# Kernel optimization log

Hardware: AMD Instinct MI355X
Metric: run time of the kernel (lower is better)

Reference implementation:

```python
import jax, jax.numpy as jnp
import numpy as np

B, T, D, H = 32, 2048, 512, 1024


def setup_inputs() -> dict:
    key = jax.random.key(0)
    ks = jax.random.split(key, 8)
    s = 1.0 / np.sqrt(H)  # torch nn.LSTM init scale
    x = jax.random.normal(ks[0], (B, T, D), jnp.float32)
    lengths = jnp.maximum(jax.random.randint(ks[1], (B,), 0, T), 1).astype(jnp.int32)
    h0 = jax.random.normal(ks[2], (1, B, H), jnp.float32)
    c0 = jax.random.normal(ks[3], (1, B, H), jnp.float32)
    W_ih = jax.random.uniform(ks[4], (4 * H, D), jnp.float32, -s, s)
    W_hh = jax.random.uniform(ks[5], (4 * H, H), jnp.float32, -s, s)
    b_ih = jax.random.uniform(ks[6], (4 * H,), jnp.float32, -s, s)
    b_hh = jax.random.uniform(ks[7], (4 * H,), jnp.float32, -s, s)
    return {"x": x, "lengths": lengths, "h0": h0, "c0": c0,
            "W_ih": W_ih, "W_hh": W_hh, "b_ih": b_ih, "b_hh": b_hh}


def _lstm_final(x, lengths, h0, c0, W_ih, W_hh, b_ih, b_hh):
    # Packed-sequence LSTM: final state per sequence == state at its last valid step.
    # Equivalent masked scan: freeze (h, c) once t >= length.
    t_len = x.shape[1]
    xt = jnp.swapaxes(x, 0, 1)                           # [T, B, D]
    mask = jnp.arange(t_len)[:, None] < lengths[None, :]  # [T, B]
    bias = b_ih + b_hh                                   # [4H]

    def step(carry, inp):
        h, c = carry                                     # [B, H] each
        xb, m = inp                                      # [B, D], [B]
        gates = xb @ W_ih.T + h @ W_hh.T + bias          # [B, 4H]
        i, f, g, o = jnp.split(gates, 4, axis=-1)        # torch gate order i,f,g,o
        c_new = jax.nn.sigmoid(f) * c + jax.nn.sigmoid(i) * jnp.tanh(g)
        h_new = jax.nn.sigmoid(o) * jnp.tanh(c_new)
        m = m[:, None]
        return (jnp.where(m, h_new, h), jnp.where(m, c_new, c)), None

    (h, c), _ = jax.lax.scan(step, (h0[0], c0[0]), (xt, mask))
    return h[None], c[None]                              # [1, B, H] each


def reference(x, lengths, h0, c0, W_ih, W_hh, b_ih, b_hh):
    return _lstm_final(x, lengths, h0, c0, W_ih, W_hh, b_ih, b_hh)
```

## Files before the change

kernel.cpp:

```cpp
#include <hip/hip_runtime.h>
#include <hip/hip_bf16.h>

#define B_ 32
#define T_ 2048
#define D_ 512
#define H_ 1024
#define G4_ 4096
#define NBLK 128
#define JPB 8
#define FSTRIDE 16

typedef __attribute__((ext_vector_type(8))) short short8;
typedef __attribute__((ext_vector_type(4))) float f32x4;
typedef __attribute__((ext_vector_type(4))) int i32x4;

__device__ __forceinline__ float sigmoidf_(float x) { return 1.0f / (1.0f + __expf(-x)); }
__device__ __forceinline__ float tanhf_(float x) {
  float e = __expf(2.0f * x);
  return 1.0f - 2.0f / (e + 1.0f);
}
__device__ __forceinline__ float bf16bits_to_f(unsigned short u) {
  return __builtin_bit_cast(float, (unsigned int)u << 16);
}
__device__ __forceinline__ unsigned short f_to_bf16bits(float f) {
  __hip_bfloat16 h = __float2bfloat16(f);
  return __builtin_bit_cast(unsigned short, h);
}

__device__ __forceinline__ i32x4 load16_sys(const void* p) {
  i32x4 v;
  asm volatile("global_load_dwordx4 %0, %1, off sc0 sc1" : "=v"(v) : "v"(p));
  return v;
}

__global__ __launch_bounds__(256) void xw_gemm(const float* __restrict__ x,
                                               const float* __restrict__ Wih,
                                               __hip_bfloat16* __restrict__ xg,
                                               int t0) {
  __shared__ __align__(16) __hip_bfloat16 As[128][40];
  __shared__ __align__(16) __hip_bfloat16 Bs[128][40];
  __shared__ __align__(16) __hip_bfloat16 Cs[128][132];

  const int tid = threadIdx.x;
  const int bx = blockIdx.x;
  const int by = blockIdx.y;
  const int lane = tid & 63, wave = tid >> 6;
  const int wm = wave >> 1, wn = wave & 1;
  const int lr = lane & 15, kq = (lane >> 4) * 8;

  const int r  = tid >> 1, ks = (tid & 1) * 16;
  const int rowA = by * 128 + r;
  const int bb = rowA & 31, tg = t0 + (rowA >> 5);
  const float* aptr = x  + ((size_t)bb * T_ + tg) * D_ + ks;
  const float* bptr = Wih + (size_t)(bx * 128 + r) * D_ + ks;

  f32x4 acc[4][4];
#pragma unroll
  for (int i = 0; i < 4; ++i)
#pragma unroll
    for (int jj = 0; jj < 4; ++jj) acc[i][jj] = (f32x4){0.f, 0.f, 0.f, 0.f};

  for (int k0 = 0; k0 < D_; k0 += 32) {
    __hip_bfloat16 ta[16], tb[16];
#pragma unroll
    for (int q = 0; q < 4; ++q) {
      f32x4 va = ((const f32x4*)(aptr + k0))[q];
      f32x4 vb = ((const f32x4*)(bptr + k0))[q];
#pragma unroll
      for (int e = 0; e < 4; ++e) {
        ta[q * 4 + e] = __float2bfloat16(va[e]);
        tb[q * 4 + e] = __float2bfloat16(vb[e]);
      }
    }
    __syncthreads();
    *(short8*)&As[r][ks]     = *(const short8*)&ta[0];
    *(short8*)&As[r][ks + 8] = *(const short8*)&ta[8];
    *(short8*)&Bs[r][ks]     = *(const short8*)&tb[0];
    *(short8*)&Bs[r][ks + 8] = *(const short8*)&tb[8];
    __syncthreads();

    short8 af[4], bf[4];
#pragma unroll
    for (int mi = 0; mi < 4; ++mi) af[mi] = *(const short8*)&As[wm * 64 + mi * 16 + lr][kq];
#pragma unroll
    for (int ni = 0; ni < 4; ++ni) bf[ni] = *(const short8*)&Bs[wn * 64 + ni * 16 + lr][kq];
#pragma unroll
    for (int mi = 0; mi < 4; ++mi)
#pragma unroll
      for (int ni = 0; ni < 4; ++ni)
        acc[mi][ni] = __builtin_amdgcn_mfma_f32_16x16x32_bf16(af[mi], bf[ni], acc[mi][ni], 0, 0, 0);
  }

#pragma unroll
  for (int mi = 0; mi < 4; ++mi)
#pragma unroll
    for (int ni = 0; ni < 4; ++ni)
#pragma unroll
      for (int rr = 0; rr < 4; ++rr)
        Cs[wm * 64 + mi * 16 + (lane >> 4) * 4 + rr][wn * 64 + ni * 16 + lr] =
            __float2bfloat16(acc[mi][ni][rr]);
  __syncthreads();

  const int orow = tid >> 1, oseg = (tid & 1) * 64;
  __hip_bfloat16* dst = xg + (size_t)(by * 128 + orow) * G4_ + bx * 128 + oseg;
#pragma unroll
  for (int c2 = 0; c2 < 8; ++c2)
    *(short8*)(dst + c2 * 8) = *(const short8*)&Cs[orow][oseg + c2 * 8];
}

__global__ __launch_bounds__(256, 1) void lstm_rec(
    const __hip_bfloat16* __restrict__ xg, const float* __restrict__ Whh,
    const int* __restrict__ lengths, const float* __restrict__ h0,
    const float* __restrict__ c0, const float* __restrict__ bih,
    const float* __restrict__ bhh, __hip_bfloat16* hbuf,
    float* __restrict__ hstate, float* __restrict__ cstate,
    int* flags, float* __restrict__ out,
    int t0, int t1, int isfirst, int islast) {
  __shared__ float Gs[4][32][36];

  const int g = blockIdx.x, tid = threadIdx.x;
  const int lane = tid & 63, w = tid >> 6;
  const int lr = lane & 15, q = lane >> 4, kq = q * 8;
  const int kkb = w * 8;

  short8 wf[2][8];
#pragma unroll
  for (int ni = 0; ni < 2; ++ni) {
    const int n2 = ni * 16 + lr;
    const int gcol = (n2 >> 3) * H_ + g * JPB + (n2 & 7);
    const float* wbase = Whh + (size_t)gcol * H_ + kq;
#pragma unroll
    for (int kk2 = 0; kk2 < 8; ++kk2) {
      const int k0 = (kkb + kk2) * 32;
      f32x4 w0 = *(const f32x4*)(wbase + k0);
      f32x4 w1 = *(const f32x4*)(wbase + k0 + 4);
      __hip_bfloat16 tw_[8];
#pragma unroll
      for (int e = 0; e < 4; ++e) { tw_[e] = __float2bfloat16(w0[e]); tw_[4 + e] = __float2bfloat16(w1[e]); }
      wf[ni][kk2] = *(const short8*)&tw_[0];
    }
  }

  const int bb2 = (tid & 127) >> 2, j2 = (tid & 3) * 2;
  const int jglob = g * JPB + j2;
  const int len_b = (tid < 128) ? lengths[bb2] : 0;
  int maxlen = 0;
  for (int p = 0; p < B_; ++p) maxlen = max(maxlen, lengths[p]);
  const int tend = min(t1, maxlen);

  float hreg[2], creg[2], bias[4][2];
  if (tid < 128) {
    if (isfirst) {
#pragma unroll
      for (int e = 0; e < 2; ++e) { hreg[e] = h0[bb2 * H_ + jglob + e]; creg[e] = c0[bb2 * H_ + jglob + e]; }
    } else {
#pragma unroll
      for (int e = 0; e < 2; ++e) { hreg[e] = hstate[bb2 * H_ + jglob + e]; creg[e] = cstate[bb2 * H_ + jglob + e]; }
    }
#pragma unroll
    for (int p = 0; p < 4; ++p)
#pragma unroll
      for (int e = 0; e < 2; ++e)
        bias[p][e] = bih[p * H_ + jglob + e] + bhh[p * H_ + jglob + e];
  }

  unsigned long long* hbuf64 = (unsigned long long*)hbuf;
  const int* myflag = &flags[(w * 32 + (lane & 31)) * FSTRIDE];
  const int pw64 = bb2 * (H_ / 4) + g * 2 + ((tid & 3) >> 1);

  for (int t = t0; t < tend; ++t) {
    unsigned int xp[4];
    if (tid < 128) {
      const __hip_bfloat16* xgrow = xg + ((size_t)(t - t0) * B_ + bb2) * G4_ + jglob;
#pragma unroll
      for (int p = 0; p < 4; ++p) xp[p] = *(const unsigned int*)(xgrow + p * H_);
    }

    while (true) {
      int f = __hip_atomic_load(myflag, __ATOMIC_RELAXED, __HIP_MEMORY_SCOPE_AGENT);
      if (__all(f >= t)) break;
      __builtin_amdgcn_s_sleep(1);
    }

    const char* hb = (const char*)(hbuf + (size_t)(t & 1) * (B_ * H_));
    i32x4 raw[2][8];
#pragma unroll
    for (int mi = 0; mi < 2; ++mi) {
      const char* rowp = hb + (size_t)(mi * 16 + lr) * (H_ * 2) + kkb * 64 + q * 16;
#pragma unroll
      for (int kk2 = 0; kk2 < 8; ++kk2)
        raw[mi][kk2] = load16_sys(rowp + kk2 * 64);
    }
    asm volatile("s_waitcnt vmcnt(0)" ::: "memory");
    __builtin_amdgcn_sched_barrier(0);

    short8 af[2][8];
#pragma unroll
    for (int mi = 0; mi < 2; ++mi)
#pragma unroll
      for (int kk2 = 0; kk2 < 8; ++kk2) {
        union { i32x4 i; short8 s; } cv;
        cv.i = raw[mi][kk2];
        af[mi][kk2] = cv.s;
      }

    f32x4 acc[2][2];
#pragma unroll
    for (int mi = 0; mi < 2; ++mi)
#pragma unroll
      for (int ni = 0; ni < 2; ++ni) acc[mi][ni] = (f32x4){0.f, 0.f, 0.f, 0.f};
#pragma unroll
    for (int kk2 = 0; kk2 < 8; ++kk2)
#pragma unroll
      for (int mi = 0; mi < 2; ++mi)
#pragma unroll
        for (int ni = 0; ni < 2; ++ni)
          acc[mi][ni] = __builtin_amdgcn_mfma_f32_16x16x32_bf16(af[mi][kk2], wf[ni][kk2], acc[mi][ni], 0, 0, 0);

#pragma unroll
    for (int mi = 0; mi < 2; ++mi)
#pragma unroll
      for (int ni = 0; ni < 2; ++ni)
#pragma unroll
        for (int rr = 0; rr < 4; ++rr)
          Gs[w][mi * 16 + q * 4 + rr][ni * 16 + lr] = acc[mi][ni][rr];
    __syncthreads();

    if (tid < 128) {
      const int upd = (t < len_b);
#pragma unroll
      for (int e = 0; e < 2; ++e) {
        const int cb = j2 + e;
        const float s0 = (Gs[0][bb2][cb]      + Gs[1][bb2][cb])      + (Gs[2][bb2][cb]      + Gs[3][bb2][cb]);
        const float s1 = (Gs[0][bb2][8 + cb]  + Gs[1][bb2][8 + cb])  + (Gs[2][bb2][8 + cb]  + Gs[3][bb2][8 + cb]);
        const float s2 = (Gs[0][bb2][16 + cb] + Gs[1][bb2][16 + cb]) + (Gs[2][bb2][16 + cb] + Gs[3][bb2][16 + cb]);
        const float s3 = (Gs[0][bb2][24 + cb] + Gs[1][bb2][24 + cb]) + (Gs[2][bb2][24 + cb] + Gs[3][bb2][24 + cb]);
        const float g0 = s0 + bf16bits_to_f((unsigned short)(xp[0] >> (16 * e))) + bias[0][e];
        const float g1 = s1 + bf16bits_to_f((unsigned short)(xp[1] >> (16 * e))) + bias[1][e];
        const float g2 = s2 + bf16bits_to_f((unsigned short)(xp[2] >> (16 * e))) + bias[2][e];
        const float g3 = s3 + bf16bits_to_f((unsigned short)(xp[3] >> (16 * e))) + bias[3][e];
        const float ig = sigmoidf_(g0), fg = sigmoidf_(g1);
        const float gg = tanhf_(g2),    og = sigmoidf_(g3);
        const float cn = fg * creg[e] + ig * gg;
        const float hn = og * tanhf_(cn);
        if (upd) { creg[e] = cn; hreg[e] = hn; }
      }
      unsigned int packed = ((unsigned int)f_to_bf16bits(hreg[1]) << 16) | f_to_bf16bits(hreg[0]);
      unsigned int other = __shfl_xor(packed, 1);
      if ((tid & 1) == 0) {
        unsigned long long w64 = ((unsigned long long)other << 32) | (unsigned long long)packed;
        __hip_atomic_store(hbuf64 + (size_t)((t + 1) & 1) * (B_ * H_ / 4) + pw64, w64,
                           __ATOMIC_RELAXED, __HIP_MEMORY_SCOPE_AGENT);
      }
    }
    __syncthreads();
    if (tid == 0)
      __hip_atomic_store(&flags[g * FSTRIDE], t + 1, __ATOMIC_RELAXED, __HIP_MEMORY_SCOPE_AGENT);
  }

  if (tid < 128) {
    if (islast) {
#pragma unroll
      for (int e = 0; e < 2; ++e) {
        out[bb2 * H_ + jglob + e] = hreg[e];
        out[B_ * H_ + bb2 * H_ + jglob + e] = creg[e];
      }
    } else {
#pragma unroll
      for (int e = 0; e < 2; ++e) {
        hstate[bb2 * H_ + jglob + e] = hreg[e];
        cstate[bb2 * H_ + jglob + e] = creg[e];
      }
    }
  }
}

__global__ void init_k(const float* __restrict__ h0, __hip_bfloat16* __restrict__ hbuf,
                       int* __restrict__ flags) {
  int i = blockIdx.x * 256 + threadIdx.x;
  if (i < B_ * H_) hbuf[i] = __float2bfloat16(h0[i]);
  if (i < NBLK * FSTRIDE) flags[i] = 0;
}

extern "C" void kernel_launch(void* const* d_in, const int* in_sizes, int n_in,
                              void* d_out, int out_size, void* d_ws, size_t ws_size,
                              hipStream_t stream) {
  const float* x       = (const float*)d_in[0];
  const int*   lengths = (const int*)d_in[1];
  const float* h0      = (const float*)d_in[2];
  const float* c0      = (const float*)d_in[3];
  const float* Wih     = (const float*)d_in[4];
  const float* Whh     = (const float*)d_in[5];
  const float* bih     = (const float*)d_in[6];
  const float* bhh     = (const float*)d_in[7];
  float* out = (float*)d_out;

  char* ws = (char*)d_ws;
  int* flags               = (int*)ws;
  __hip_bfloat16* hbuf     = (__hip_bfloat16*)(ws + 8192);
  float* hstate            = (float*)(ws + 8192 + 131072);
  float* cstate            = (float*)(ws + 8192 + 262144);
  __hip_bfloat16* xg       = (__hip_bfloat16*)(ws + 524288);

  size_t avail = (ws_size > 524288) ? ws_size - 524288 : 0;
  int tc = (int)(avail / ((size_t)B_ * G4_ * 2));
  if (tc > T_) tc = T_;
  tc &= ~3;
  if (tc < 4) tc = 4;

  hipLaunchKernelGGL(init_k, dim3(128), dim3(256), 0, stream, h0, hbuf, flags);
  for (int t0 = 0; t0 < T_; t0 += tc) {
    int len = min(tc, T_ - t0);
    dim3 gg(G4_ / 128, (len * B_) / 128);
    hipLaunchKernelGGL(xw_gemm, gg, dim3(256), 0, stream, x, Wih, xg, t0);
    hipLaunchKernelGGL(lstm_rec, dim3(NBLK), dim3(256), 0, stream,
                       xg, Whh, lengths, h0, c0, bih, bhh, hbuf, hstate, cstate,
                       flags, out, t0, t0 + len, (t0 == 0) ? 1 : 0,
                       (t0 + len >= T_) ? 1 : 0);
  }
}
```

Measured before the change: 9.474 ms.

## Halve recurrent blocks to 64 with 512 threads and 16 hidden units each

```diff
diff --git a/kernel.cpp b/kernel.cpp
--- a/kernel.cpp
+++ b/kernel.cpp
@@ -6,9 +6,8 @@
 #define D_ 512
 #define H_ 1024
 #define G4_ 4096
-#define NBLK 128
-#define JPB 8
-#define FSTRIDE 16
+#define NBLK 64
+#define JPB 16
 
 typedef __attribute__((ext_vector_type(8))) short short8;
 typedef __attribute__((ext_vector_type(4))) float f32x4;
@@ -31,6 +30,9 @@
   i32x4 v;
   asm volatile("global_load_dwordx4 %0, %1, off sc0 sc1" : "=v"(v) : "v"(p));
   return v;
+}
+__device__ __forceinline__ void store16_sys(void* p, i32x4 v) {
+  asm volatile("global_store_dwordx4 %0, %1, off sc0 sc1" :: "v"(p), "v"(v) : "memory");
 }
 
 __global__ __launch_bounds__(256) void xw_gemm(const float* __restrict__ x,
@@ -108,7 +110,7 @@
     *(short8*)(dst + c2 * 8) = *(const short8*)&Cs[orow][oseg + c2 * 8];
 }
 
-__global__ __launch_bounds__(256, 1) void lstm_rec(
+__global__ __launch_bounds__(512, 1) void lstm_rec(
     const __hip_bfloat16* __restrict__ xg, const float* __restrict__ Whh,
     const int* __restrict__ lengths, const float* __restrict__ h0,
     const float* __restrict__ c0, const float* __restrict__ bih,
@@ -116,21 +118,21 @@
     float* __restrict__ hstate, float* __restrict__ cstate,
     int* flags, float* __restrict__ out,
     int t0, int t1, int isfirst, int islast) {
-  __shared__ float Gs[4][32][36];
+  __shared__ float Gs[8][33][70];
 
   const int g = blockIdx.x, tid = threadIdx.x;
   const int lane = tid & 63, w = tid >> 6;
   const int lr = lane & 15, q = lane >> 4, kq = q * 8;
-  const int kkb = w * 8;
-
-  short8 wf[2][8];
-#pragma unroll
-  for (int ni = 0; ni < 2; ++ni) {
-    const int n2 = ni * 16 + lr;
-    const int gcol = (n2 >> 3) * H_ + g * JPB + (n2 & 7);
+  const int kkb = w * 4;
+
+  short8 wf[4][4];
+#pragma unroll
+  for (int ni = 0; ni < 4; ++ni) {
+    const int n = ni * 16 + lr;
+    const int gcol = (n >> 4) * H_ + g * JPB + (n & 15);
     const float* wbase = Whh + (size_t)gcol * H_ + kq;
 #pragma unroll
-    for (int kk2 = 0; kk2 < 8; ++kk2) {
+    for (int kk2 = 0; kk2 < 4; ++kk2) {
       const int k0 = (kkb + kk2) * 32;
       f32x4 w0 = *(const f32x4*)(wbase + k0);
       f32x4 w1 = *(const f32x4*)(wbase + k0 + 4);
@@ -141,137 +143,120 @@
     }
   }
 
-  const int bb2 = (tid & 127) >> 2, j2 = (tid & 3) * 2;
-  const int jglob = g * JPB + j2;
-  const int len_b = (tid < 128) ? lengths[bb2] : 0;
+  const int bb2 = tid >> 4, j1 = tid & 15;
+  const int jglob = g * JPB + j1;
+  const int len_b = lengths[bb2];
   int maxlen = 0;
   for (int p = 0; p < B_; ++p) maxlen = max(maxlen, lengths[p]);
   const int tend = min(t1, maxlen);
 
-  float hreg[2], creg[2], bias[4][2];
-  if (tid < 128) {
-    if (isfirst) {
-#pragma unroll
-      for (int e = 0; e < 2; ++e) { hreg[e] = h0[bb2 * H_ + jglob + e]; creg[e] = c0[bb2 * H_ + jglob + e]; }
-    } else {
-#pragma unroll
-      for (int e = 0; e < 2; ++e) { hreg[e] = hstate[bb2 * H_ + jglob + e]; creg[e] = cstate[bb2 * H_ + jglob + e]; }
-    }
-#pragma unroll
-    for (int p = 0; p < 4; ++p)
-#pragma unroll
-      for (int e = 0; e < 2; ++e)
-        bias[p][e] = bih[p * H_ + jglob + e] + bhh[p * H_ + jglob + e];
-  }
-
-  unsigned long long* hbuf64 = (unsigned long long*)hbuf;
-  const int* myflag = &flags[(w * 32 + (lane & 31)) * FSTRIDE];
-  const int pw64 = bb2 * (H_ / 4) + g * 2 + ((tid & 3) >> 1);
+  float hreg, creg, bias[4];
+  if (isfirst) { hreg = h0[bb2 * H_ + jglob]; creg = c0[bb2 * H_ + jglob]; }
+  else         { hreg = hstate[bb2 * H_ + jglob]; creg = cstate[bb2 * H_ + jglob]; }
+#pragma unroll
+  for (int p = 0; p < 4; ++p) bias[p] = bih[p * H_ + jglob] + bhh[p * H_ + jglob];
+
+  const int* myflag = &flags[w * 8 + (lane & 7)];
+  char* const hstore_base = (char*)hbuf;
+  const size_t poff = (size_t)bb2 * (H_ * 2) + g * (JPB * 2) + ((tid >> 3) & 1) * 16;
 
   for (int t = t0; t < tend; ++t) {
-    unsigned int xp[4];
-    if (tid < 128) {
+    float xv[4];
+    {
       const __hip_bfloat16* xgrow = xg + ((size_t)(t - t0) * B_ + bb2) * G4_ + jglob;
 #pragma unroll
-      for (int p = 0; p < 4; ++p) xp[p] = *(const unsigned int*)(xgrow + p * H_);
+      for (int p = 0; p < 4; ++p) xv[p] = __bfloat162float(xgrow[p * H_]);
     }
 
     while (true) {
       int f = __hip_atomic_load(myflag, __ATOMIC_RELAXED, __HIP_MEMORY_SCOPE_AGENT);
-      if (__all(f >= t)) break;
+      if (__all((lane >= 8) || (f >= t))) break;
       __builtin_amdgcn_s_sleep(1);
     }
 
     const char* hb = (const char*)(hbuf + (size_t)(t & 1) * (B_ * H_));
-    i32x4 raw[2][8];
+    i32x4 raw[2][4];
 #pragma unroll
     for (int mi = 0; mi < 2; ++mi) {
       const char* rowp = hb + (size_t)(mi * 16 + lr) * (H_ * 2) + kkb * 64 + q * 16;
 #pragma unroll
-      for (int kk2 = 0; kk2 < 8; ++kk2)
+      for (int kk2 = 0; kk2 < 4; ++kk2)
         raw[mi][kk2] = load16_sys(rowp + kk2 * 64);
     }
     asm volatile("s_waitcnt vmcnt(0)" ::: "memory");
     __builtin_amdgcn_sched_barrier(0);
 
-    short8 af[2][8];
+    short8 af[2][4];
 #pragma unroll
     for (int mi = 0; mi < 2; ++mi)
 #pragma unroll
-      for (int kk2 = 0; kk2 < 8; ++kk2) {
+      for (int kk2 = 0; kk2 < 4; ++kk2) {
         union { i32x4 i; short8 s; } cv;
         cv.i = raw[mi][kk2];
         af[mi][kk2] = cv.s;
       }
 
-    f32x4 acc[2][2];
+    f32x4 acc[2][4];
 #pragma unroll
     for (int mi = 0; mi < 2; ++mi)
 #pragma unroll
-      for (int ni = 0; ni < 2; ++ni) acc[mi][ni] = (f32x4){0.f, 0.f, 0.f, 0.f};
-#pragma unroll
-    for (int kk2 = 0; kk2 < 8; ++kk2)
+      for (int ni = 0; ni < 4; ++ni) acc[mi][ni] = (f32x4){0.f, 0.f, 0.f, 0.f};
+#pragma unroll
+    for (int kk2 = 0; kk2 < 4; ++kk2)
 #pragma unroll
       for (int mi = 0; mi < 2; ++mi)
 #pragma unroll
-        for (int ni = 0; ni < 2; ++ni)
+        for (int ni = 0; ni < 4; ++ni)
           acc[mi][ni] = __builtin_amdgcn_mfma_f32_16x16x32_bf16(af[mi][kk2], wf[ni][kk2], acc[mi][ni], 0, 0, 0);
 
 #pragma unroll
     for (int mi = 0; mi < 2; ++mi)
 #pragma unroll
-      for (int ni = 0; ni < 2; ++ni)
+      for (int ni = 0; ni < 4; ++ni)
 #pragma unroll
         for (int rr = 0; rr < 4; ++rr)
           Gs[w][mi * 16 + q * 4 + rr][ni * 16 + lr] = acc[mi][ni][rr];
     __syncthreads();
 
-    if (tid < 128) {
+    {
       const int upd = (t < len_b);
-#pragma unroll
-      for (int e = 0; e < 2; ++e) {
-        const int cb = j2 + e;
-        const float s0 = (Gs[0][bb2][cb]      + Gs[1][bb2][cb])      + (Gs[2][bb2][cb]      + Gs[3][bb2][cb]);
-        const float s1 = (Gs[0][bb2][8 + cb]  + Gs[1][bb2][8 + cb])  + (Gs[2][bb2][8 + cb]  + Gs[3][bb2][8 + cb]);
-        const float s2 = (Gs[0][bb2][16 + cb] + Gs[1][bb2][16 + cb]) + (Gs[2][bb2][16 + cb] + Gs[3][bb2][16 + cb]);
-        const float s3 = (Gs[0][bb2][24 + cb] + Gs[1][bb2][24 + cb]) + (Gs[2][bb2][24 + cb] + Gs[3][bb2][24 + cb]);
-        const float g0 = s0 + bf16bits_to_f((unsigned short)(xp[0] >> (16 * e))) + bias[0][e];
-        const float g1 = s1 + bf16bits_to_f((unsigned short)(xp[1] >> (16 * e))) + bias[1][e];
-        const float g2 = s2 + bf16bits_to_f((unsigned short)(xp[2] >> (16 * e))) + bias[2][e];
-        const float g3 = s3 + bf16bits_to_f((unsigned short)(xp[3] >> (16 * e))) + bias[3][e];
-        const float ig = sigmoidf_(g0), fg = sigmoidf_(g1);
-        const float gg = tanhf_(g2),    og = sigmoidf_(g3);
-        const float cn = fg * creg[e] + ig * gg;
-        const float hn = og * tanhf_(cn);
-        if (upd) { creg[e] = cn; hreg[e] = hn; }
+      float s[4];
+#pragma unroll
+      for (int p = 0; p < 4; ++p) {
+        const int cb = p * 16 + j1;
+        s[p] = ((Gs[0][bb2][cb] + Gs[1][bb2][cb]) + (Gs[2][bb2][cb] + Gs[3][bb2][cb])) +
+               ((Gs[4][bb2][cb] + Gs[5][bb2][cb]) + (Gs[6][bb2][cb] + Gs[7][bb2][cb]));
       }
-      unsigned int packed = ((unsigned int)f_to_bf16bits(hreg[1]) << 16) | f_to_bf16bits(hreg[0]);
-      unsigned int other = __shfl_xor(packed, 1);
-      if ((tid & 1) == 0) {
-        unsigned long long w64 = ((unsigned long long)other << 32) | (unsigned long long)packed;
-        __hip_atomic_store(hbuf64 + (size_t)((t + 1) & 1) * (B_ * H_ / 4) + pw64, w64,
-                           __ATOMIC_RELAXED, __HIP_MEMORY_SCOPE_AGENT);
+      const float ig = sigmoidf_(s[0] + xv[0] + bias[0]);
+      const float fg = sigmoidf_(s[1] + xv[1] + bias[1]);
+      const float gg = tanhf_(s[2] + xv[2] + bias[2]);
+      const float og = sigmoidf_(s[3] + xv[3] + bias[3]);
+      const float cn = fg * creg + ig * gg;
+      const float hn = og * tanhf_(cn);
+      if (upd) { creg = cn; hreg = hn; }
+
+      unsigned int hb16 = (unsigned int)f_to_bf16bits(hreg);
+      unsigned int a01 = (hb16 & 0xFFFFu) | (__shfl_xor(hb16, 1) << 16);
+      unsigned int a23 = __shfl_xor(a01, 2);
+      unsigned int a45 = __shfl_xor(a01, 4);
+      unsigned int a67 = __shfl_xor(a23, 4);
+      if ((tid & 7) == 0) {
+        i32x4 v; v[0] = (int)a01; v[1] = (int)a23; v[2] = (int)a45; v[3] = (int)a67;
+        store16_sys(hstore_base + (size_t)((t + 1) & 1) * (B_ * H_ * 2) + poff, v);
+        asm volatile("s_waitcnt vmcnt(0)" ::: "memory");
       }
     }
     __syncthreads();
     if (tid == 0)
-      __hip_atomic_store(&flags[g * FSTRIDE], t + 1, __ATOMIC_RELAXED, __HIP_MEMORY_SCOPE_AGENT);
-  }
-
-  if (tid < 128) {
-    if (islast) {
-#pragma unroll
-      for (int e = 0; e < 2; ++e) {
-        out[bb2 * H_ + jglob + e] = hreg[e];
-        out[B_ * H_ + bb2 * H_ + jglob + e] = creg[e];
-      }
-    } else {
-#pragma unroll
-      for (int e = 0; e < 2; ++e) {
-        hstate[bb2 * H_ + jglob + e] = hreg[e];
-        cstate[bb2 * H_ + jglob + e] = creg[e];
-      }
-    }
+      __hip_atomic_store(&flags[g], t + 1, __ATOMIC_RELAXED, __HIP_MEMORY_SCOPE_AGENT);
+  }
+
+  if (islast) {
+    out[bb2 * H_ + jglob] = hreg;
+    out[B_ * H_ + bb2 * H_ + jglob] = creg;
+  } else {
+    hstate[bb2 * H_ + jglob] = hreg;
+    cstate[bb2 * H_ + jglob] = creg;
   }
 }
 
@@ -279,7 +264,7 @@
                        int* __restrict__ flags) {
   int i = blockIdx.x * 256 + threadIdx.x;
   if (i < B_ * H_) hbuf[i] = __float2bfloat16(h0[i]);
-  if (i < NBLK * FSTRIDE) flags[i] = 0;
+  if (i < NBLK) flags[i] = 0;
 }
 
 extern "C" void kernel_launch(void* const* d_in, const int* in_sizes, int n_in,
@@ -313,7 +298,7 @@
     int len = min(tc, T_ - t0);
     dim3 gg(G4_ / 128, (len * B_) / 128);
     hipLaunchKernelGGL(xw_gemm, gg, dim3(256), 0, stream, x, Wih, xg, t0);
-    hipLaunchKernelGGL(lstm_rec, dim3(NBLK), dim3(256), 0, stream,
+    hipLaunchKernelGGL(lstm_rec, dim3(NBLK), dim3(512), 0, stream,
                        xg, Whh, lengths, h0, c0, bih, bhh, hbuf, hstate, cstate,
                        flags, out, t0, t0 + len, (t0 == 0) ? 1 : 0,
                        (t0 + len >= T_) ? 1 : 0);
```

Result: slower. 12.35 ms (+30.3%).
